# Kernel tuning notes

Measured on AMD Instinct MI355X. Metric: run time of the kernel, lower is better.

The kernel has to match this reference:

```python
import jax, jax.numpy as jnp
import numpy as np

B, T, D, V, CD, NF = 2, 2048, 1024, 32000, 1024, 4
EPS_NORM = 1e-12
EPS_LN = 1e-5


def _gelu(x):
    return jax.nn.gelu(x, approximate=False)


def _l2norm(x):
    n = jnp.linalg.norm(x, axis=-1, keepdims=True)
    return x / jnp.maximum(n, EPS_NORM)


def setup_inputs() -> dict:
    key = jax.random.key(0)
    ks = jax.random.split(key, 24)
    s = 0.02
    inp = {
        "tokens": jax.random.randint(ks[0], (B, T), 0, V),
        "c_states": jax.random.normal(ks[1], (8, CD), dtype=jnp.float32),
        "embed": jax.random.normal(ks[2], (V, D), dtype=jnp.float32) * s,
        "pos_embed": jax.random.normal(ks[3], (T, D), dtype=jnp.float32) * s,
        # c_to_topo: Linear(c_dim,64) -> GELU -> Linear(64,2) -> Softplus (dead code in fwd, kept for completeness)
        "topo_W1": jax.random.normal(ks[4], (CD, 64), dtype=jnp.float32) * s,
        "topo_b1": jnp.zeros((64,), jnp.float32),
        "topo_W2": jax.random.normal(ks[5], (64, 2), dtype=jnp.float32) * s,
        "topo_b2": jnp.zeros((2,), jnp.float32),
        # c_to_thresh: Linear(c_dim,32) -> GELU -> Linear(32,NF) -> Sigmoid
        "thr_W1": jax.random.normal(ks[6], (CD, 32), dtype=jnp.float32) * s,
        "thr_b1": jnp.zeros((32,), jnp.float32),
        "thr_W2": jax.random.normal(ks[7], (32, NF), dtype=jnp.float32) * s,
        "thr_b2": jnp.zeros((NF,), jnp.float32),
        # simplex layers: NF x (Linear(2D,D) -> GELU -> Linear(D,D))
        "simp_W1": jax.random.normal(ks[8], (NF, 2 * D, D), dtype=jnp.float32) * s,
        "simp_b1": jnp.zeros((NF, D), jnp.float32),
        "simp_W2": jax.random.normal(ks[9], (NF, D, D), dtype=jnp.float32) * s,
        "simp_b2": jnp.zeros((NF, D), jnp.float32),
        # topo_integrate: Linear(D+2, 2D) -> GELU -> Linear(2D, D)
        "int_W1": jax.random.normal(ks[10], (D + 2, 2 * D), dtype=jnp.float32) * s,
        "int_b1": jnp.zeros((2 * D,), jnp.float32),
        "int_W2": jax.random.normal(ks[11], (2 * D, D), dtype=jnp.float32) * s,
        "int_b2": jnp.zeros((D,), jnp.float32),
        "ln_g": jnp.ones((D,), jnp.float32),
        "ln_b": jnp.zeros((D,), jnp.float32),
        "head_W": jax.random.normal(ks[12], (D, V), dtype=jnp.float32) * s,
    }
    return inp


def _forward(tokens, c_states, embed, pos_embed,
             topo_W1, topo_b1, topo_W2, topo_b2,
             thr_W1, thr_b1, thr_W2, thr_b2,
             simp_W1, simp_b1, simp_W2, simp_b2,
             int_W1, int_b1, int_W2, int_b2,
             ln_g, ln_b, head_W):
    b, t = tokens.shape
    x = embed[tokens] + pos_embed[jnp.arange(t)][None]          # [B,T,D]
    c_pooled = c_states.mean(axis=0)                            # [CD]
    thresholds = jax.nn.sigmoid(_gelu(c_pooled @ thr_W1 + thr_b1) @ thr_W2 + thr_b2)  # [NF]

    for level in range(NF):
        thresh = thresholds[level]
        x0 = x[0]                                               # [T,D] (module only uses batch elem 0)
        xn = _l2norm(x0)
        sim = xn @ xn.T                                         # [T,T]
        adj = jax.nn.sigmoid(10.0 * (sim - thresh))
        agg = adj @ x0                                          # dense message aggregation
        combined = jnp.concatenate([x0, agg], axis=-1)          # [T,2D]
        update = _gelu(combined @ simp_W1[level] + simp_b1[level]) @ simp_W2[level] + simp_b2[level]
        x = x + update[None] * 0.2                              # broadcast update across batch

    # approximate Betti numbers on detached embeddings
    xd = jax.lax.stop_gradient(x[0])
    xn = _l2norm(xd)
    sim = xn @ xn.T
    adj = jax.nn.sigmoid(10.0 * (sim - 0.5))
    degree = adj.sum(axis=-1)
    beta0 = (degree < 0.5).astype(jnp.float32).sum()
    n_edges = adj.sum() / 2.0
    beta1 = jax.nn.relu(n_edges - jnp.float32(t) + beta0 + 1.0)
    betti = jnp.stack([beta0, beta1])                           # [2]
    betti_exp = jnp.broadcast_to(betti[None, None, :], (b, t, 2))

    x = jnp.concatenate([x, betti_exp], axis=-1)                # [B,T,D+2]
    x = _gelu(x @ int_W1 + int_b1) @ int_W2 + int_b2            # [B,T,D]
    mu = x.mean(axis=-1, keepdims=True)
    var = x.var(axis=-1, keepdims=True)
    x = (x - mu) / jnp.sqrt(var + EPS_LN) * ln_g + ln_b
    return x @ head_W                                           # [B,T,V]


def reference(tokens, c_states, embed, pos_embed,
              topo_W1, topo_b1, topo_W2, topo_b2,
              thr_W1, thr_b1, thr_W2, thr_b2,
              simp_W1, simp_b1, simp_W2, simp_b2,
              int_W1, int_b1, int_W2, int_b2,
              ln_g, ln_b, head_W):
    return _forward(tokens, c_states, embed, pos_embed,
                    topo_W1, topo_b1, topo_W2, topo_b2,
                    thr_W1, thr_b1, thr_W2, thr_b2,
                    simp_W1, simp_b1, simp_W2, simp_b2,
                    int_W1, int_b1, int_W2, int_b2,
                    ln_g, ln_b, head_W)
```

## Files before the change

kernel.cpp:

```cpp
#include <hip/hip_runtime.h>

typedef __bf16 bf16;
using bf16x8 = __attribute__((ext_vector_type(8))) __bf16;
using bf16x4 = __attribute__((ext_vector_type(4))) __bf16;
using f32x4  = __attribute__((ext_vector_type(4))) float;

#define DEV __device__ __forceinline__
#define SCHED_FENCE() __builtin_amdgcn_sched_barrier(0)

DEV float gelu_f(float x){ return 0.5f*x*(1.0f+erff(x*0.7071067811865475f)); }
DEV float sigm_f(float x){ return 1.0f/(1.0f+expf(-x)); }

DEV void gload16(const bf16* g, bf16* l){
    __builtin_amdgcn_global_load_lds(
        (const __attribute__((address_space(1))) void*)g,
        (__attribute__((address_space(3))) void*)l, 16, 0, 0);
}

enum { EPI_ADJ=0, EPI_BF16=1, EPI_GELU_BIAS=2, EPI_XUPD=3, EPI_BIAS_F32=4, EPI_F32=5 };

template<int BM,int BN,int WM,int WN,int EPI>
__global__ __launch_bounds__(WM*WN*64, 2)
void gemm_p(const bf16* __restrict__ A, const bf16* __restrict__ B,
            int M, int N, int K, void* __restrict__ Cout, int ldc,
            const float* __restrict__ bias, const float* __restrict__ scal, int sidx,
            float* __restrict__ xu0, float* __restrict__ xu1)
{
    constexpr int THREADS = WM*WN*64;
    constexpr int MR = BM/WM/16, NR = BN/WN/16;
    constexpr int ATILE = BM*64, BTILE = BN*64;
    constexpr int RR = THREADS/8;
    constexpr int VM = (BM+BN)/RR;
    __shared__ bf16 sm[2*(ATILE+BTILE)];

    const int nbm = M/BM, nbn = N/BN;
    const int nwg = nbm*nbn;
    int wg = blockIdx.x;
    wg = (wg&7)*(nwg>>3) + (wg>>3);
    const int by = wg % nbm, bx = wg / nbm;
    const int tid = threadIdx.x, lane = tid&63, wid = tid>>6;
    const int wm = wid / WN, wn = wid % WN;
    const int fr = lane&15, fq = lane>>4;

    const bf16* Ab = A + (long)(by*BM + (tid>>3))*K + (((tid&7) ^ ((tid>>3)&7))<<3);
    const bf16* Bb = B + (long)(bx*BN + (tid>>3))*K + (((tid&7) ^ ((tid>>3)&7))<<3);

    auto STAGE = [&](int tt, int cb){
        bf16* d = sm + cb*(ATILE+BTILE) + wid*512;
        const long ko = (long)tt*64;
#pragma unroll
        for (int g=0; g<BM/RR; ++g)
            gload16(Ab + (long)g*RR*K + ko, d + g*RR*64);
#pragma unroll
        for (int g=0; g<BN/RR; ++g)
            gload16(Bb + (long)g*RR*K + ko, d + ATILE + g*RR*64);
    };

    f32x4 acc[MR][NR] = {};
    const int nt = K >> 6;

    STAGE(0,0);
    STAGE(1,1);

    for (int t=0; t<nt; ++t){
        const bf16* bufA = sm + (t&1)*(ATILE+BTILE);
        const bf16* bufB = bufA + ATILE;
        if (t+1<nt){
            if constexpr (VM==6)      asm volatile("s_waitcnt vmcnt(6)" ::: "memory");
            else if constexpr (VM==8) asm volatile("s_waitcnt vmcnt(8)" ::: "memory");
            else                      asm volatile("s_waitcnt vmcnt(0)" ::: "memory");
        } else {
            asm volatile("s_waitcnt vmcnt(0)" ::: "memory");
        }
        __builtin_amdgcn_s_barrier();
        __builtin_amdgcn_sched_barrier(0);
#pragma unroll
        for (int ks=0; ks<2; ++ks){
            bf16x8 af[MR], bv[NR];
            const int ch = (((ks*4+fq) ^ (fr&7))<<3);
#pragma unroll
            for (int j=0;j<MR;++j)
                af[j] = *(const bf16x8*)&bufA[(wm*(MR*16) + j*16 + fr)*64 + ch];
#pragma unroll
            for (int j=0;j<NR;++j)
                bv[j] = *(const bf16x8*)&bufB[(wn*(NR*16) + j*16 + fr)*64 + ch];
            __builtin_amdgcn_s_setprio(1);
#pragma unroll
            for (int mi=0;mi<MR;++mi)
#pragma unroll
            for (int ni=0;ni<NR;++ni)
                acc[mi][ni] = __builtin_amdgcn_mfma_f32_16x16x32_bf16(
                    af[mi], bv[ni], acc[mi][ni], 0,0,0);
            __builtin_amdgcn_s_setprio(0);
        }
        asm volatile("s_waitcnt lgkmcnt(0)" ::: "memory");
        __builtin_amdgcn_s_barrier();
        if (t+2<nt) STAGE(t+2, t&1);
    }

    float thr = 0.f;
    if constexpr (EPI==EPI_ADJ) thr = scal[sidx];

#pragma unroll
    for (int mi=0;mi<MR;++mi){
#pragma unroll
        for (int ni=0;ni<NR;++ni){
            const int col = bx*BN + wn*(NR*16) + ni*16 + fr;
#pragma unroll
            for (int r=0;r<4;++r){
                const int row = by*BM + wm*(MR*16) + mi*16 + fq*4 + r;
                const float v = acc[mi][ni][r];
                const long ci = (long)row*ldc + col;
                if constexpr (EPI==EPI_ADJ)       ((bf16*)Cout)[ci] = (bf16)sigm_f(10.f*(v - thr));
                else if constexpr (EPI==EPI_BF16) ((bf16*)Cout)[ci] = (bf16)v;
                else if constexpr (EPI==EPI_GELU_BIAS) ((bf16*)Cout)[ci] = (bf16)gelu_f(v + bias[col]);
                else if constexpr (EPI==EPI_BIAS_F32)  ((float*)Cout)[ci] = v + bias[col];
                else if constexpr (EPI==EPI_F32)       ((float*)Cout)[ci] = v;
                else if constexpr (EPI==EPI_XUPD){
                    const float u = 0.2f*(v + bias[col]);
                    xu0[ci] += u;  xu1[ci] += u;
                }
            }
        }
    }
}

template<int EPI>
__global__ __launch_bounds__(512, 2)
void gemm8(const bf16* __restrict__ A, const bf16* __restrict__ B,
           int M, int N, int K, void* __restrict__ Cout, int ldc,
           const float* __restrict__ bias)
{
    __shared__ bf16 sm[65536];
    const int nbm = M>>8, nbn = N>>8;
    const int nwg = nbm*nbn;
    int wg = blockIdx.x;
    wg = (wg&7)*(nwg>>3) + (wg>>3);
    const int by = wg % nbm, bx = wg / nbm;
    const int tid = threadIdx.x, lane = tid&63, wid = tid>>6;
    const int wm = wid>>2, wn = wid&3;
    const int fr = lane&15, fq = lane>>4;

    const bf16* Ag = A + (long)(by*256 + (tid>>3))*K + (((tid&7) ^ ((tid>>3)&7))<<3);
    const bf16* Bg = B + (long)(bx*256 + (tid>>3))*K + (((tid&7) ^ ((tid>>3)&7))<<3);

    auto SA = [&](int tt, int h){
        bf16* d = sm + (tt&1)*32768 + wid*512;
        const long ko = (long)tt*64;
        gload16(Ag + (long)(h*64)*K + ko,       d + h*4096);
        gload16(Ag + (long)(128+h*64)*K + ko,   d + 8192 + h*4096);
    };
    auto SB = [&](int tt, int h){
        bf16* d = sm + (tt&1)*32768 + 16384 + wid*512;
        const long ko = (long)tt*64;
#pragma unroll
        for (int g=0; g<2; ++g)
            gload16(Bg + (long)(h*2+g)*64*K + ko, d + (h*2+g)*4096);
    };

    f32x4 acc[8][4] = {};
    bf16x8 aCur[8], b0[4], b1[4];
    const int nt = K >> 6;

    SA(0,0); SB(0,0); SA(0,1); SB(0,1);
    SA(1,0); SB(1,0); SA(1,1);
    SCHED_FENCE();

    for (int t=0; t<nt; ++t){
        const bf16* bufA = sm + (t&1)*32768;
        const bf16* bufB = bufA + 16384;

        auto LDA = [&](int mh){
#pragma unroll
            for (int ks=0;ks<2;++ks){
                const int ch = (((ks*4+fq) ^ (fr&7))<<3);
#pragma unroll
                for (int j=0;j<4;++j)
                    aCur[ks*4+j] = *(const bf16x8*)&bufA[(wm*128 + mh*64 + j*16 + fr)*64 + ch];
            }
        };
        auto LDB = [&](int nh, bf16x8* dst){
#pragma unroll
            for (int ks=0;ks<2;++ks){
                const int ch = (((ks*4+fq) ^ (fr&7))<<3);
#pragma unroll
                for (int j=0;j<2;++j)
                    dst[ks*2+j] = *(const bf16x8*)&bufB[(wn*64 + nh*32 + j*16 + fr)*64 + ch];
            }
        };
        auto QMFMA = [&](int mh, int nh, bf16x8* bArr){
            __builtin_amdgcn_s_setprio(1);
#pragma unroll
            for (int ks=0;ks<2;++ks)
#pragma unroll
            for (int j=0;j<4;++j)
#pragma unroll
            for (int jj=0;jj<2;++jj)
                acc[mh*4+j][nh*2+jj] = __builtin_amdgcn_mfma_f32_16x16x32_bf16(
                    aCur[ks*4+j], bArr[ks*2+jj], acc[mh*4+j][nh*2+jj], 0,0,0);
            __builtin_amdgcn_s_setprio(0);
            SCHED_FENCE();
        };

        if (t+1<nt) asm volatile("s_waitcnt vmcnt(6)" ::: "memory");
        else        asm volatile("s_waitcnt vmcnt(0)" ::: "memory");
        __builtin_amdgcn_s_barrier();
        SCHED_FENCE();
        if (t+1<nt) SB(t+1,1);
        SCHED_FENCE();
        LDA(0); LDB(0, b0);
        asm volatile("s_waitcnt lgkmcnt(0)" ::: "memory");
        SCHED_FENCE();
        QMFMA(0,0,b0);
        __builtin_amdgcn_s_barrier();
        SCHED_FENCE();
        if (t+2<nt) SA(t+2,0);
        SCHED_FENCE();
        LDB(1, b1);
        asm volatile("s_waitcnt lgkmcnt(0)" ::: "memory");
        SCHED_FENCE();
        QMFMA(0,1,b1);
        __builtin_amdgcn_s_barrier();
        SCHED_FENCE();
        if (t+2<nt) SB(t+2,0);
        SCHED_FENCE();
        LDA(1);
        asm volatile("s_waitcnt lgkmcnt(0)" ::: "memory");
        SCHED_FENCE();
        QMFMA(1,1,b1);
        __builtin_amdgcn_s_barrier();
        SCHED_FENCE();
        if (t+2<nt) SA(t+2,1);
        SCHED_FENCE();
        QMFMA(1,0,b0);
    }

#pragma unroll
    for (int mi=0;mi<8;++mi){
#pragma unroll
        for (int ni=0;ni<4;++ni){
            const int col = bx*256 + wn*64 + ni*16 + fr;
#pragma unroll
            for (int r=0;r<4;++r){
                const int row = by*256 + wm*128 + mi*16 + fq*4 + r;
                const float v = acc[mi][ni][r];
                const long ci = (long)row*ldc + col;
                if constexpr (EPI==EPI_F32)            ((float*)Cout)[ci] = v;
                else if constexpr (EPI==EPI_BIAS_F32)  ((float*)Cout)[ci] = v + bias[col];
                else                                   ((bf16*)Cout)[ci] = (bf16)v;
            }
        }
    }
}

__global__ void prep_kernel(const float* __restrict__ cs,
                            const float* __restrict__ W1, const float* __restrict__ b1,
                            const float* __restrict__ W2, const float* __restrict__ b2,
                            float* __restrict__ thrs)
{
    __shared__ float cp[1024];
    __shared__ float part[8][32];
    __shared__ float h[32];
    const int tid = threadIdx.x;
    for (int j = tid; j < 1024; j += 256){
        float s = 0.f;
#pragma unroll
        for (int r = 0; r < 8; r++) s += cs[r*1024 + j];
        cp[j] = s * 0.125f;
    }
    __syncthreads();
    const int t = tid & 31, g = tid >> 5;
    float p = 0.f;
    for (int j = g*128; j < g*128+128; j++) p += cp[j] * W1[j*32 + t];
    part[g][t] = p;
    __syncthreads();
    if (tid < 32){
        float s = b1[tid];
#pragma unroll
        for (int q=0;q<8;q++) s += part[q][tid];
        h[tid] = gelu_f(s);
    }
    __syncthreads();
    if (tid < 4){
        float z = b2[tid];
        for (int k=0;k<32;k++) z += h[k]*W2[k*4 + tid];
        thrs[tid] = sigm_f(z);
    }
    if (tid == 4) thrs[4] = 0.5f;
}

__global__ void embed_kernel(const int* __restrict__ tok, const float* __restrict__ emb,
                             const float* __restrict__ pos, float* __restrict__ x)
{
    const long i = (long)blockIdx.x*256 + threadIdx.x;
    const int  d4 = i & 255;
    const long bt = i >> 8;
    const int  t  = (int)(bt & 2047);
    const int  token = tok[bt];
    f32x4 e = *(const f32x4*)(emb + (long)token*1024 + d4*4);
    f32x4 p = *(const f32x4*)(pos + (long)t*1024 + d4*4);
    *(f32x4*)(x + i*4) = e + p;
}

__global__ void transpose_f2b(const float* __restrict__ in, int ldin,
                              bf16* __restrict__ out, int ldout, int R, int C)
{
    __shared__ float tile[32][33];
    const int nbx = C >> 5;
    const int bx = blockIdx.x % nbx, by = blockIdx.x / nbx;
    const int tx = threadIdx.x & 31, ty = threadIdx.x >> 5;
#pragma unroll
    for (int i=0;i<32;i+=8)
        tile[ty+i][tx] = in[(long)(by*32+ty+i)*ldin + bx*32+tx];
    __syncthreads();
#pragma unroll
    for (int i=0;i<32;i+=8)
        out[(long)(bx*32+ty+i)*ldout + by*32+tx] = (bf16)tile[tx][ty+i];
}

__global__ void rownorm_kernel(const float* __restrict__ x, bf16* __restrict__ xn,
                               bf16* __restrict__ x0b, int ld0)
{
    const long t = blockIdx.x; const int tid = threadIdx.x;
    f32x4 v = *(const f32x4*)(x + t*1024 + tid*4);
    float s = v.x*v.x + v.y*v.y + v.z*v.z + v.w*v.w;
#pragma unroll
    for (int o=32;o>0;o>>=1) s += __shfl_down(s, o);
    __shared__ float red[4];
    if ((tid&63)==0) red[tid>>6] = s;
    __syncthreads();
    const float tot = red[0]+red[1]+red[2]+red[3];
    const float inv = 1.0f / fmaxf(sqrtf(tot), 1e-12f);
    bf16x4 a, b;
    a[0]=(bf16)(v.x*inv); a[1]=(bf16)(v.y*inv); a[2]=(bf16)(v.z*inv); a[3]=(bf16)(v.w*inv);
    b[0]=(bf16)v.x; b[1]=(bf16)v.y; b[2]=(bf16)v.z; b[3]=(bf16)v.w;
    *(bf16x4*)(xn  + t*1024 + tid*4) = a;
    *(bf16x4*)(x0b + t*ld0  + tid*4) = b;
}

__global__ void degree_kernel(const bf16* __restrict__ adj, float* __restrict__ deg)
{
    const long t = blockIdx.x; const int tid = threadIdx.x;
    bf16x8 v = *(const bf16x8*)(adj + t*2048 + tid*8);
    float s = 0.f;
#pragma unroll
    for (int j=0;j<8;j++) s += (float)v[j];
#pragma unroll
    for (int o=32;o>0;o>>=1) s += __shfl_down(s, o);
    __shared__ float red[4];
    if ((tid&63)==0) red[tid>>6] = s;
    __syncthreads();
    if (tid==0) deg[t] = red[0]+red[1]+red[2]+red[3];
}

__global__ void betti_kernel(const float* __restrict__ deg, float* __restrict__ betti)
{
    const int tid = threadIdx.x;
    float s = 0.f, c = 0.f;
#pragma unroll
    for (int i=0;i<8;i++){
        const float d = deg[tid*8 + i];
        s += d;  c += (d < 0.5f) ? 1.f : 0.f;
    }
#pragma unroll
    for (int o=32;o>0;o>>=1){ s += __shfl_down(s,o); c += __shfl_down(c,o); }
    __shared__ float ss[4], cc[4];
    if ((tid&63)==0){ ss[tid>>6]=s; cc[tid>>6]=c; }
    __syncthreads();
    if (tid==0){
        const float S = ss[0]+ss[1]+ss[2]+ss[3];
        const float C = cc[0]+cc[1]+cc[2]+cc[3];
        const float ne = 0.5f*S;
        const float b1 = ne - 2048.f + C + 1.f;
        betti[0] = C;
        betti[1] = b1 > 0.f ? b1 : 0.f;
    }
}

__global__ void b1eff_kernel(const float* __restrict__ ib1, const float* __restrict__ iW1,
                             const float* __restrict__ betti, float* __restrict__ out)
{
    const int j = blockIdx.x*256 + threadIdx.x;
    out[j] = ib1[j] + betti[0]*iW1[(long)1024*2048 + j] + betti[1]*iW1[(long)1025*2048 + j];
}

__global__ void f2b_kernel(const float* __restrict__ in, bf16* __restrict__ out)
{
    const long i = (long)blockIdx.x*256 + threadIdx.x;
    f32x4 a = *(const f32x4*)(in + i*8);
    f32x4 c = *(const f32x4*)(in + i*8 + 4);
    bf16x8 o;
    o[0]=(bf16)a.x; o[1]=(bf16)a.y; o[2]=(bf16)a.z; o[3]=(bf16)a.w;
    o[4]=(bf16)c.x; o[5]=(bf16)c.y; o[6]=(bf16)c.z; o[7]=(bf16)c.w;
    *(bf16x8*)(out + i*8) = o;
}

__global__ void ln_kernel(const float* __restrict__ y, const float* __restrict__ g,
                          const float* __restrict__ b, bf16* __restrict__ out)
{
    const long t = blockIdx.x; const int tid = threadIdx.x;
    f32x4 v = *(const f32x4*)(y + t*1024 + tid*4);
    float s  = v.x+v.y+v.z+v.w;
    float s2 = v.x*v.x+v.y*v.y+v.z*v.z+v.w*v.w;
#pragma unroll
    for (int o=32;o>0;o>>=1){ s += __shfl_down(s,o); s2 += __shfl_down(s2,o); }
    __shared__ float ss[4], qq[4];
    if ((tid&63)==0){ ss[tid>>6]=s; qq[tid>>6]=s2; }
    __syncthreads();
    const float S = ss[0]+ss[1]+ss[2]+ss[3], Q = qq[0]+qq[1]+qq[2]+qq[3];
    const float mu  = S * (1.f/1024.f);
    const float var = Q * (1.f/1024.f) - mu*mu;
    const float inv = rsqrtf(var + 1e-5f);
    f32x4 gv = *(const f32x4*)(g + tid*4);
    f32x4 bv = *(const f32x4*)(b + tid*4);
    bf16x4 o;
    o[0] = (bf16)((v.x - mu)*inv*gv.x + bv.x);
    o[1] = (bf16)((v.y - mu)*inv*gv.y + bv.y);
    o[2] = (bf16)((v.z - mu)*inv*gv.z + bv.z);
    o[3] = (bf16)((v.w - mu)*inv*gv.w + bv.w);
    *(bf16x4*)(out + t*1024 + tid*4) = o;
}

extern "C" void kernel_launch(void* const* d_in, const int* in_sizes, int n_in,
                              void* d_out, int out_size, void* d_ws, size_t ws_size,
                              hipStream_t stream)
{
    const int*   tokens = (const int*)  d_in[0];
    const float* cstate = (const float*)d_in[1];
    const float* embedW = (const float*)d_in[2];
    const float* posW   = (const float*)d_in[3];
    const float* thrW1  = (const float*)d_in[8];
    const float* thrb1  = (const float*)d_in[9];
    const float* thrW2  = (const float*)d_in[10];
    const float* thrb2  = (const float*)d_in[11];
    const float* simpW1 = (const float*)d_in[12];
    const float* simpb1 = (const float*)d_in[13];
    const float* simpW2 = (const float*)d_in[14];
    const float* simpb2 = (const float*)d_in[15];
    const float* intW1  = (const float*)d_in[16];
    const float* intb1  = (const float*)d_in[17];
    const float* intW2  = (const float*)d_in[18];
    const float* intb2  = (const float*)d_in[19];
    const float* lng    = (const float*)d_in[20];
    const float* lnb    = (const float*)d_in[21];
    const float* headW  = (const float*)d_in[22];
    float* out = (float*)d_out;

    size_t off = 0;
    auto carve = [&](size_t bytes) -> void* {
        void* p = (char*)d_ws + off;
        off += (bytes + 255) & ~(size_t)255;
        return p;
    };
    float* x_f32   = (float*)carve(16777216);
    bf16*  xn      = (bf16*) carve(4194304);
    bf16*  x0T     = (bf16*) carve(4194304);
    bf16*  comb    = (bf16*) carve(8388608);
    bf16*  adj     = (bf16*) carve(8388608);
    bf16*  h1      = (bf16*) carve(4194304);
    bf16*  xb      = (bf16*) carve(8388608);
    bf16*  w1T     = (bf16*) carve(16777216);
    bf16*  w2T     = (bf16*) carve(8388608);
    bf16*  i1T     = (bf16*) carve(4194304);
    bf16*  i2T     = (bf16*) carve(4194304);
    bf16*  hT      = (bf16*) carve(65536000);
    float* degree  = (float*)carve(8192);
    float* b1eff   = (float*)carve(8192);
    float* thrs    = (float*)carve(64);
    float* betti   = (float*)carve(64);
    bf16*  h2  = comb;
    float* yv  = x_f32;
    bf16*  xln = xn;

    const dim3 blk(256);
    const dim3 blk512(512);

    prep_kernel<<<1, blk, 0, stream>>>(cstate, thrW1, thrb1, thrW2, thrb2, thrs);
    embed_kernel<<<4096, blk, 0, stream>>>(tokens, embedW, posW, x_f32);

    for (int l=0;l<4;l++)
        transpose_f2b<<<(1024/32)*(2048/32), blk, 0, stream>>>(
            simpW1 + (long)l*2048*1024, 1024, w1T + (long)l*1024*2048, 2048, 2048, 1024);
    for (int l=0;l<4;l++)
        transpose_f2b<<<(1024/32)*(1024/32), blk, 0, stream>>>(
            simpW2 + (long)l*1024*1024, 1024, w2T + (long)l*1024*1024, 1024, 1024, 1024);
    transpose_f2b<<<(2048/32)*(1024/32), blk, 0, stream>>>(intW1, 2048, i1T, 1024, 1024, 2048);
    transpose_f2b<<<(1024/32)*(2048/32), blk, 0, stream>>>(intW2, 1024, i2T, 2048, 2048, 1024);
    transpose_f2b<<<(32000/32)*(1024/32), blk, 0, stream>>>(headW, 32000, hT, 1024, 1024, 32000);

    for (int l=0;l<4;l++){
        rownorm_kernel<<<2048, blk, 0, stream>>>(x_f32, xn, comb, 2048);
        transpose_f2b<<<(1024/32)*(2048/32), blk, 0, stream>>>(x_f32, 1024, x0T, 2048, 2048, 1024);
        gemm_p<128,128,2,2,EPI_ADJ><<<16*16, blk, 0, stream>>>(
            xn, xn, 2048, 2048, 1024, adj, 2048, nullptr, thrs, l, nullptr, nullptr);
        gemm_p<64,128,2,2,EPI_BF16><<<32*8, blk, 0, stream>>>(
            adj, x0T, 2048, 1024, 2048, comb + 1024, 2048, nullptr, nullptr, 0, nullptr, nullptr);
        gemm_p<64,128,2,2,EPI_GELU_BIAS><<<32*8, blk, 0, stream>>>(
            comb, w1T + (long)l*1024*2048, 2048, 1024, 2048, h1, 1024,
            simpb1 + l*1024, nullptr, 0, nullptr, nullptr);
        gemm_p<64,128,2,2,EPI_XUPD><<<32*8, blk, 0, stream>>>(
            h1, w2T + (long)l*1024*1024, 2048, 1024, 1024, nullptr, 1024,
            simpb2 + l*1024, nullptr, 0, x_f32, x_f32 + (long)2048*1024);
    }

    rownorm_kernel<<<2048, blk, 0, stream>>>(x_f32, xn, comb, 2048);
    gemm_p<128,128,2,2,EPI_ADJ><<<16*16, blk, 0, stream>>>(
        xn, xn, 2048, 2048, 1024, adj, 2048, nullptr, thrs, 4, nullptr, nullptr);
    degree_kernel<<<2048, blk, 0, stream>>>(adj, degree);
    betti_kernel<<<1, blk, 0, stream>>>(degree, betti);
    b1eff_kernel<<<8, blk, 0, stream>>>(intb1, intW1, betti, b1eff);

    f2b_kernel<<<2048, blk, 0, stream>>>(x_f32, xb);
    gemm_p<128,128,2,2,EPI_GELU_BIAS><<<32*16, blk, 0, stream>>>(
        xb, i1T, 4096, 2048, 1024, h2, 2048, b1eff, nullptr, 0, nullptr, nullptr);
    gemm_p<128,128,2,2,EPI_BIAS_F32><<<32*8, blk, 0, stream>>>(
        h2, i2T, 4096, 1024, 2048, yv, 1024, intb2, nullptr, 0, nullptr, nullptr);
    ln_kernel<<<4096, blk, 0, stream>>>(yv, lng, lnb, xln);
    gemm8<EPI_F32><<<16*125, blk512, 0, stream>>>(
        xln, hT, 4096, 32000, 1024, out, 32000, nullptr);
}
```

Before: 880.4 us.

## Batch weight transposes, raise occupancy hint, reorder head GEMM tile mapping

Merges the per-layer weight transpose launches into one batched launch each, using a layer stride. Raises the min-blocks-per-SM launch bound from 2 to 3 on the 64x128 GEMMs so more workgroups can be resident. Changes the head GEMM's workgroup-to-tile mapping so consecutive groups walk along N instead of M, which alters L2 reuse of the activation and weight tiles. The occupancy hint may force register spills, and the new mapping may reduce reuse of the large head weight.

```diff
diff --git a/kernel.cpp b/kernel.cpp
--- a/kernel.cpp
+++ b/kernel.cpp
@@ -19,8 +19,8 @@
 
 enum { EPI_ADJ=0, EPI_BF16=1, EPI_GELU_BIAS=2, EPI_XUPD=3, EPI_BIAS_F32=4, EPI_F32=5 };
 
-template<int BM,int BN,int WM,int WN,int EPI>
-__global__ __launch_bounds__(WM*WN*64, 2)
+template<int BM,int BN,int WM,int WN,int MINW,int EPI>
+__global__ __launch_bounds__(WM*WN*64, MINW)
 void gemm_p(const bf16* __restrict__ A, const bf16* __restrict__ B,
             int M, int N, int K, void* __restrict__ Cout, int ldc,
             const float* __restrict__ bias, const float* __restrict__ scal, int sidx,
@@ -136,7 +136,7 @@
     const int nwg = nbm*nbn;
     int wg = blockIdx.x;
     wg = (wg&7)*(nwg>>3) + (wg>>3);
-    const int by = wg % nbm, bx = wg / nbm;
+    const int bx = wg % nbn, by = wg / nbn;
     const int tid = threadIdx.x, lane = tid&63, wid = tid>>6;
     const int wm = wid>>2, wn = wid&3;
     const int fr = lane&15, fq = lane>>4;
@@ -302,20 +302,26 @@
     *(f32x4*)(x + i*4) = e + p;
 }
 
-__global__ void transpose_f2b(const float* __restrict__ in, int ldin,
-                              bf16* __restrict__ out, int ldout, int R, int C)
+__global__ void transpose_f2b(const float* __restrict__ in, int ldin, long istr,
+                              bf16* __restrict__ out, int ldout, long ostr,
+                              int R, int C)
 {
     __shared__ float tile[32][33];
-    const int nbx = C >> 5;
-    const int bx = blockIdx.x % nbx, by = blockIdx.x / nbx;
+    const int nbx = C >> 5, nby = R >> 5;
+    const int per = nbx*nby;
+    const int l  = blockIdx.x / per;
+    const int rm = blockIdx.x % per;
+    const int bx = rm % nbx, by = rm / nbx;
+    const float* inl = in + (long)l*istr;
+    bf16* outl = out + (long)l*ostr;
     const int tx = threadIdx.x & 31, ty = threadIdx.x >> 5;
 #pragma unroll
     for (int i=0;i<32;i+=8)
-        tile[ty+i][tx] = in[(long)(by*32+ty+i)*ldin + bx*32+tx];
+        tile[ty+i][tx] = inl[(long)(by*32+ty+i)*ldin + bx*32+tx];
     __syncthreads();
 #pragma unroll
     for (int i=0;i<32;i+=8)
-        out[(long)(bx*32+ty+i)*ldout + by*32+tx] = (bf16)tile[tx][ty+i];
+        outl[(long)(bx*32+ty+i)*ldout + by*32+tx] = (bf16)tile[tx][ty+i];
 }
 
 __global__ void rownorm_kernel(const float* __restrict__ x, bf16* __restrict__ xn,
@@ -478,42 +484,44 @@
     prep_kernel<<<1, blk, 0, stream>>>(cstate, thrW1, thrb1, thrW2, thrb2, thrs);
     embed_kernel<<<4096, blk, 0, stream>>>(tokens, embedW, posW, x_f32);
 
-    for (int l=0;l<4;l++)
-        transpose_f2b<<<(1024/32)*(2048/32), blk, 0, stream>>>(
-            simpW1 + (long)l*2048*1024, 1024, w1T + (long)l*1024*2048, 2048, 2048, 1024);
-    for (int l=0;l<4;l++)
-        transpose_f2b<<<(1024/32)*(1024/32), blk, 0, stream>>>(
-            simpW2 + (long)l*1024*1024, 1024, w2T + (long)l*1024*1024, 1024, 1024, 1024);
-    transpose_f2b<<<(2048/32)*(1024/32), blk, 0, stream>>>(intW1, 2048, i1T, 1024, 1024, 2048);
-    transpose_f2b<<<(1024/32)*(2048/32), blk, 0, stream>>>(intW2, 1024, i2T, 2048, 2048, 1024);
-    transpose_f2b<<<(32000/32)*(1024/32), blk, 0, stream>>>(headW, 32000, hT, 1024, 1024, 32000);
+    transpose_f2b<<<4*(1024/32)*(2048/32), blk, 0, stream>>>(
+        simpW1, 1024, (long)2048*1024, w1T, 2048, (long)1024*2048, 2048, 1024);
+    transpose_f2b<<<4*(1024/32)*(1024/32), blk, 0, stream>>>(
+        simpW2, 1024, (long)1024*1024, w2T, 1024, (long)1024*1024, 1024, 1024);
+    transpose_f2b<<<(2048/32)*(1024/32), blk, 0, stream>>>(
+        intW1, 2048, 0, i1T, 1024, 0, 1024, 2048);
+    transpose_f2b<<<(1024/32)*(2048/32), blk, 0, stream>>>(
+        intW2, 1024, 0, i2T, 2048, 0, 2048, 1024);
+    transpose_f2b<<<(32000/32)*(1024/32), blk, 0, stream>>>(
+        headW, 32000, 0, hT, 1024, 0, 1024, 32000);
 
     for (int l=0;l<4;l++){
         rownorm_kernel<<<2048, blk, 0, stream>>>(x_f32, xn, comb, 2048);
-        transpose_f2b<<<(1024/32)*(2048/32), blk, 0, stream>>>(x_f32, 1024, x0T, 2048, 2048, 1024);
-        gemm_p<128,128,2,2,EPI_ADJ><<<16*16, blk, 0, stream>>>(
+        transpose_f2b<<<(1024/32)*(2048/32), blk, 0, stream>>>(
+            x_f32, 1024, 0, x0T, 2048, 0, 2048, 1024);
+        gemm_p<128,128,2,2,2,EPI_ADJ><<<16*16, blk, 0, stream>>>(
             xn, xn, 2048, 2048, 1024, adj, 2048, nullptr, thrs, l, nullptr, nullptr);
-        gemm_p<64,128,2,2,EPI_BF16><<<32*8, blk, 0, stream>>>(
+        gemm_p<64,128,2,2,3,EPI_BF16><<<32*8, blk, 0, stream>>>(
             adj, x0T, 2048, 1024, 2048, comb + 1024, 2048, nullptr, nullptr, 0, nullptr, nullptr);
-        gemm_p<64,128,2,2,EPI_GELU_BIAS><<<32*8, blk, 0, stream>>>(
+        gemm_p<64,128,2,2,3,EPI_GELU_BIAS><<<32*8, blk, 0, stream>>>(
             comb, w1T + (long)l*1024*2048, 2048, 1024, 2048, h1, 1024,
             simpb1 + l*1024, nullptr, 0, nullptr, nullptr);
-        gemm_p<64,128,2,2,EPI_XUPD><<<32*8, blk, 0, stream>>>(
+        gemm_p<64,128,2,2,3,EPI_XUPD><<<32*8, blk, 0, stream>>>(
             h1, w2T + (long)l*1024*1024, 2048, 1024, 1024, nullptr, 1024,
             simpb2 + l*1024, nullptr, 0, x_f32, x_f32 + (long)2048*1024);
     }
 
     rownorm_kernel<<<2048, blk, 0, stream>>>(x_f32, xn, comb, 2048);
-    gemm_p<128,128,2,2,EPI_ADJ><<<16*16, blk, 0, stream>>>(
+    gemm_p<128,128,2,2,2,EPI_ADJ><<<16*16, blk, 0, stream>>>(
         xn, xn, 2048, 2048, 1024, adj, 2048, nullptr, thrs, 4, nullptr, nullptr);
     degree_kernel<<<2048, blk, 0, stream>>>(adj, degree);
     betti_kernel<<<1, blk, 0, stream>>>(degree, betti);
     b1eff_kernel<<<8, blk, 0, stream>>>(intb1, intW1, betti, b1eff);
 
     f2b_kernel<<<2048, blk, 0, stream>>>(x_f32, xb);
-    gemm_p<128,128,2,2,EPI_GELU_BIAS><<<32*16, blk, 0, stream>>>(
+    gemm_p<128,128,2,2,2,EPI_GELU_BIAS><<<32*16, blk, 0, stream>>>(
         xb, i1T, 4096, 2048, 1024, h2, 2048, b1eff, nullptr, 0, nullptr, nullptr);
-    gemm_p<128,128,2,2,EPI_BIAS_F32><<<32*8, blk, 0, stream>>>(
+    gemm_p<128,128,2,2,2,EPI_BIAS_F32><<<32*8, blk, 0, stream>>>(
         h2, i2T, 4096, 1024, 2048, yv, 1024, intb2, nullptr, 0, nullptr, nullptr);
     ln_kernel<<<4096, blk, 0, stream>>>(yv, lng, lnb, xln);
     gemm8<EPI_F32><<<16*125, blk512, 0, stream>>>(
```

Measured after the change: 862.1 us. 2.1% less time.
